# Kernel tuning notes

Hardware: AMD Instinct MI355X
Metric: run time of the kernel (lower is better)

The kernel has to match this reference:

```python
import jax, jax.numpy as jnp
import numpy as np

B, T, D = 2, 1024, 384
d = D // 3            # 128
D3 = 3 * d            # 384
D9 = 9 * d            # 1152
GAMMA = 5.0
EPS_W = 1e-8
EPS_N = 1e-5


def _orth(rng, n):
    q, _ = np.linalg.qr(rng.standard_normal((n, n)).astype(np.float64))
    return jnp.asarray(q.astype(np.float32))


def setup_inputs() -> dict:
    key = jax.random.key(0)
    x = jax.random.normal(key, (B, T, D), dtype=jnp.float32)
    rng = np.random.default_rng(0)
    def plin(fan_in, fan_out):
        W = jnp.asarray(rng.standard_normal((fan_out, fan_in)).astype(np.float32) * 0.05)
        b = jnp.zeros((fan_out,), jnp.float32)
        return W, b
    Wq, bq = plin(d, D3); Sq = _orth(rng, D3)
    Wk, bk = plin(d, D3); Sk = _orth(rng, D3)
    Wv, bv = plin(d, D3); Sv = _orth(rng, D3)
    Wp, bp = plin(D3, D9)
    gn = jnp.ones((D9,), jnp.float32)
    bn = jnp.zeros((D9,), jnp.float32)
    return {"x": x, "Wq": Wq, "bq": bq, "Sq": Sq, "Wk": Wk, "bk": bk, "Sk": Sk,
            "Wv": Wv, "bv": bv, "Sv": Sv, "Wp": Wp, "bp": bp, "gn": gn, "bn": bn}


def _plin(x, W, b):
    # PositiveLinearHK: linear with softplus-positive weights
    return x @ jax.nn.softplus(W).T + b


def reference(x, Wq, bq, Sq, Wk, bk, Sk, Wv, bv, Sv, Wp, bp, gn, bn):
    Q_base = x[:, :, 0 * d:1 * d]
    K_base = x[:, :, 1 * d:2 * d]
    V_base = x[:, :, 2 * d:3 * d]
    # proj = PositiveLinearHK -> SingleStiefelProjector (orthogonal mixing)
    Q = _plin(Q_base, Wq, bq) @ Sq          # (B,T,3d)
    K = _plin(K_base, Wk, bk) @ Sk
    V = _plin(V_base, Wv, bv) @ Sv
    dots = jnp.einsum('bti,btj->btij', Q, K)            # (B,T,3d,3d)
    scores = jax.nn.sigmoid(GAMMA * dots)
    weights = scores / (scores.sum(axis=-1, keepdims=True) + EPS_W)
    attended = jnp.einsum('btij,btj->bti', weights, V)  # (B,T,3d)
    h = _plin(attended, Wp, bp)                         # (B,T,9d)
    mu = h.mean(axis=-1, keepdims=True)
    var = h.var(axis=-1, keepdims=True)
    return (h - mu) * jax.lax.rsqrt(var + EPS_N) * gn + bn
```

## Files before the change

kernel.cpp:

```cpp
#include <hip/hip_runtime.h>
#include <hip/hip_bf16.h>
#include <math.h>

#define NTOK  2048
#define DD    128
#define DD3   384
#define DD9   1152
#define TB    2
#define TBP   8
#define GAMMA_F 5.0f
#define LN2_F   0.69314718f

#define OFF_M    0
#define OFF_C    147456
#define OFF_BP   148608
#define OFF_ATT  369792
#define OFF_SSUM 763008

typedef __attribute__((ext_vector_type(2))) float f32x2;
typedef __attribute__((ext_vector_type(8))) short bf16x8;
typedef __attribute__((ext_vector_type(4))) float f32x4;

__device__ __forceinline__ float softplusf(float x) {
    return fmaxf(x, 0.0f) + log1pf(__expf(-fabsf(x)));
}
__device__ __forceinline__ unsigned short f2bf(float f) {
    __hip_bfloat16 h = __float2bfloat16(f);
    return *reinterpret_cast<unsigned short*>(&h);
}
__device__ __forceinline__ float bf2f(unsigned short u) {
    return __uint_as_float(((unsigned)u) << 16);
}

__global__ __launch_bounds__(384) void k_prep(const float* __restrict__ Wq, const float* __restrict__ Wk,
                                              const float* __restrict__ Wv, const float* __restrict__ Wp,
                                              const float* __restrict__ Sq, const float* __restrict__ Sk,
                                              const float* __restrict__ Sv, const float* __restrict__ bq,
                                              const float* __restrict__ bk, const float* __restrict__ bv,
                                              float* __restrict__ ws) {
    __shared__ float sw[DD3];
    int b = blockIdx.x, tid = threadIdx.x;
    if (b < 576) {
        int idx = b * 384 + tid;
        unsigned lo = f2bf(softplusf(Wp[2 * idx + 0]) - LN2_F);
        unsigned hi = f2bf(softplusf(Wp[2 * idx + 1]) - LN2_F);
        ((unsigned*)(ws + OFF_BP))[idx] = lo | (hi << 16);
    } else if (b < 960) {
        int bb = b - 576;
        int mat = bb >> 7, i = bb & 127;
        const float* W = (mat == 0) ? Wq : (mat == 1 ? Wk : Wv);
        const float* S = (mat == 0) ? Sq : (mat == 1 ? Sk : Sv);
        int m = tid;
        sw[m] = softplusf(W[m * DD + i]);
        __syncthreads();
        const float4* sw4 = (const float4*)sw;
        float a0 = 0.f, a1 = 0.f, a2 = 0.f, a3 = 0.f;
        for (int j4 = 0; j4 < 96; ++j4) {
            float4 w = sw4[j4];
            int j = j4 * 4;
            a0 = fmaf(w.x, S[(j + 0) * DD3 + m], a0);
            a1 = fmaf(w.y, S[(j + 1) * DD3 + m], a1);
            a2 = fmaf(w.z, S[(j + 2) * DD3 + m], a2);
            a3 = fmaf(w.w, S[(j + 3) * DD3 + m], a3);
        }
        ws[OFF_M + mat * 49152 + (i >> 2) * (DD3 * 4) + m * 4 + (i & 3)] = (a0 + a1) + (a2 + a3);
    } else {
        int mat = b - 960;
        const float* S = (mat == 0) ? Sq : (mat == 1 ? Sk : Sv);
        const float* bb_ = (mat == 0) ? bq : (mat == 1 ? bk : bv);
        int m = tid;
        float a0 = 0.f, a1 = 0.f, a2 = 0.f, a3 = 0.f;
        for (int j4 = 0; j4 < 96; ++j4) {
            int j = j4 * 4;
            a0 = fmaf(bb_[j + 0], S[(j + 0) * DD3 + m], a0);
            a1 = fmaf(bb_[j + 1], S[(j + 1) * DD3 + m], a1);
            a2 = fmaf(bb_[j + 2], S[(j + 2) * DD3 + m], a2);
            a3 = fmaf(bb_[j + 3], S[(j + 3) * DD3 + m], a3);
        }
        ws[OFF_C + mat * DD3 + m] = (a0 + a1) + (a2 + a3);
    }
}

#define PSIG(FQ2, K2, V2, RS2, AV2) do {                                      \
        f32x2 x_ = __builtin_elementwise_min(                                  \
                     __builtin_elementwise_max((FQ2) * (K2), NEG1), POS1);     \
        f32x2 w_ = x_ * x_;                                                    \
        f32x2 p_ = __builtin_elementwise_fma(                                  \
                   __builtin_elementwise_fma(                                  \
                   __builtin_elementwise_fma(                                  \
                   __builtin_elementwise_fma(                                  \
                   __builtin_elementwise_fma(                                  \
                   __builtin_elementwise_fma(PC13, w_, PC11),                  \
                     w_, PC9), w_, PC7), w_, PC5), w_, PC3), w_, PC1);         \
        f32x2 s_ = __builtin_elementwise_fma(x_, p_, HALF2);                   \
        RS2 = RS2 + s_;                                                        \
        AV2 = __builtin_elementwise_fma(s_, (V2), AV2);                        \
    } while (0)

__global__ __launch_bounds__(384, 6) void k_attn(const float* __restrict__ x,
                                                 float* __restrict__ ws) {
    __shared__ float qkv[3 * TB * DD3];
    __shared__ float att[TB * DD3];
    __shared__ float red[16];

    int tid = threadIdx.x;
    int tok0 = blockIdx.x * TB;
    const float* xb = x + (size_t)tok0 * DD3;

#pragma unroll
    for (int mat = 0; mat < 3; ++mat) {
        const float4* M4 = (const float4*)(ws + OFF_M + mat * 49152);
        const float* xt0 = xb + 0 * DD3 + mat * DD;
        const float* xt1 = xb + 1 * DD3 + mat * DD;
        float a0 = 0.f, a1 = 0.f;
        for (int i4 = 0; i4 < 32; ++i4) {
            float4 mm = M4[i4 * DD3 + tid];
            int i = i4 * 4;
            a0 = fmaf(xt0[i], mm.x, fmaf(xt0[i + 1], mm.y, fmaf(xt0[i + 2], mm.z, fmaf(xt0[i + 3], mm.w, a0))));
            a1 = fmaf(xt1[i], mm.x, fmaf(xt1[i + 1], mm.y, fmaf(xt1[i + 2], mm.z, fmaf(xt1[i + 3], mm.w, a1))));
        }
        float c = ws[OFF_C + mat * DD3 + tid];
        qkv[(mat * TB + 0) * DD3 + tid] = a0 + c;
        qkv[(mat * TB + 1) * DD3 + tid] = a1 + c;
    }
    __syncthreads();

    {
        const f32x2 NEG1  = (f32x2){-1.0f, -1.0f};
        const f32x2 POS1  = (f32x2){ 1.0f,  1.0f};
        const f32x2 HALF2 = (f32x2){ 0.5f,  0.5f};
        const f32x2 PC1   = (f32x2){  1.4919730f,   1.4919730f};
        const f32x2 PC3   = (f32x2){ -4.1350490f,  -4.1350490f};
        const f32x2 PC5   = (f32x2){ 10.9501565f,  10.9501565f};
        const f32x2 PC7   = (f32x2){-20.0847165f, -20.0847165f};
        const f32x2 PC9   = (f32x2){ 22.6396415f,  22.6396415f};
        const f32x2 PC11  = (f32x2){-13.8982400f, -13.8982400f};
        const f32x2 PC13  = (f32x2){  3.5340290f,   3.5340290f};

        int t  = tid / 192;
        int ts = tid - t * 192;
        const float* Qt = qkv + t * DD3;
        float fq0s = Qt[ts]       * (GAMMA_F / 6.0f);
        float fq1s = Qt[ts + 192] * (GAMMA_F / 6.0f);
        f32x2 fq0 = (f32x2){fq0s, fq0s};
        f32x2 fq1 = (f32x2){fq1s, fq1s};
        const float4* K4 = (const float4*)(qkv + (TB + t) * DD3);
        const float4* V4 = (const float4*)(qkv + (2 * TB + t) * DD3);
        f32x2 rs0 = (f32x2){0.f, 0.f}, rs1 = (f32x2){0.f, 0.f};
        f32x2 av0 = (f32x2){0.f, 0.f}, av1 = (f32x2){0.f, 0.f};
        for (int j4 = 0; j4 < 96; ++j4) {
            float4 kk = K4[j4];
            float4 vv = V4[j4];
            f32x2 kxy = (f32x2){kk.x, kk.y}, kzw = (f32x2){kk.z, kk.w};
            f32x2 vxy = (f32x2){vv.x, vv.y}, vzw = (f32x2){vv.z, vv.w};
            PSIG(fq0, kxy, vxy, rs0, av0);
            PSIG(fq0, kzw, vzw, rs0, av0);
            PSIG(fq1, kxy, vxy, rs1, av1);
            PSIG(fq1, kzw, vzw, rs1, av1);
        }
        float a0 = (av0.x + av0.y) * __builtin_amdgcn_rcpf(rs0.x + rs0.y + 1e-8f);
        float a1 = (av1.x + av1.y) * __builtin_amdgcn_rcpf(rs1.x + rs1.y + 1e-8f);
        unsigned short b0 = f2bf(a0), b1 = f2bf(a1);
        att[t * DD3 + ts]       = bf2f(b0);
        att[t * DD3 + ts + 192] = bf2f(b1);
        unsigned short* ag = (unsigned short*)(ws + OFF_ATT);
        ag[(size_t)(tok0 + t) * DD3 + ts]       = b0;
        ag[(size_t)(tok0 + t) * DD3 + ts + 192] = b1;
    }
    __syncthreads();

    int wave = tid >> 6, lane64 = tid & 63;
    float s0 = att[0 * DD3 + tid];
    float s1 = att[1 * DD3 + tid];
#pragma unroll
    for (int off = 32; off; off >>= 1) {
        s0 += __shfl_down(s0, off, 64);
        s1 += __shfl_down(s1, off, 64);
    }
    if (lane64 == 0) { red[wave] = s0; red[8 + wave] = s1; }
    __syncthreads();
    if (tid < TB) {
        float a = 0.f;
        for (int w = 0; w < 6; ++w) a += red[tid * 8 + w];
        ws[OFF_SSUM + tok0 + tid] = a;
    }
}

__global__ __launch_bounds__(384) void k_proj(const float* __restrict__ bp,
                                              const float* __restrict__ gn,
                                              const float* __restrict__ bn,
                                              const float* __restrict__ ws,
                                              float* __restrict__ out) {
    __shared__ unsigned short attb[16 * 392];
    __shared__ float h[TBP * DD9];
    __shared__ float red[64];
    __shared__ float smu[TBP], sinv[TBP];

    int tid = threadIdx.x;
    int wave = tid >> 6, lane64 = tid & 63;
    int tok0 = blockIdx.x * TBP;

    {
        const unsigned short* ag = (const unsigned short*)(ws + OFF_ATT) + (size_t)tok0 * DD3;
        int r = tid / 48, c = (tid - r * 48) * 8;
        *(uint4*)(attb + r * 392 + c) = *(const uint4*)(ag + tid * 8);
        uint4 z; z.x = z.y = z.z = z.w = 0u;
        *(uint4*)(attb + (8 + r) * 392 + c) = z;
    }
    __syncthreads();

    {
        int n0w  = wave * 192;
        int brow = lane64 & 15;
        int koff = (lane64 >> 4) * 8;
        const unsigned short* Bp = (const unsigned short*)(ws + OFF_BP);
        const unsigned short* abase = attb + brow * 392 + koff;
        const unsigned short* bbase = Bp + (size_t)(n0w + brow) * DD3 + koff;
        f32x4 acc[12];
#pragma unroll
        for (int nt = 0; nt < 12; ++nt) acc[nt] = (f32x4){0.f, 0.f, 0.f, 0.f};
        for (int ks = 0; ks < 12; ++ks) {
            bf16x8 a = *(const bf16x8*)(abase + ks * 32);
            const unsigned short* bk_ = bbase + ks * 32;
#pragma unroll
            for (int nt = 0; nt < 12; ++nt) {
                bf16x8 bfr = *(const bf16x8*)(bk_ + nt * 16 * DD3);
                acc[nt] = __builtin_amdgcn_mfma_f32_16x16x32_bf16(a, bfr, acc[nt], 0, 0, 0);
            }
        }
        if (lane64 < 32) {
            int rbase = (lane64 >> 4) * 4;
            int col0  = n0w + (lane64 & 15);
#pragma unroll
            for (int nt = 0; nt < 12; ++nt) {
#pragma unroll
                for (int r = 0; r < 4; ++r)
                    h[(rbase + r) * DD9 + col0 + nt * 16] = acc[nt][r];
            }
        }
    }
    __syncthreads();

    const float* ssums = ws + OFF_SSUM + tok0;
    float acc3[3][TBP];
    {
        float bp0 = bp[tid], bp1 = bp[tid + DD3], bp2 = bp[tid + 2 * DD3];
#pragma unroll
        for (int t = 0; t < TBP; ++t) {
            float base = LN2_F * ssums[t];
            acc3[0][t] = h[t * DD9 + tid]           + bp0 + base;
            acc3[1][t] = h[t * DD9 + tid + DD3]     + bp1 + base;
            acc3[2][t] = h[t * DD9 + tid + 2 * DD3] + bp2 + base;
        }
    }
#pragma unroll
    for (int t = 0; t < TBP; ++t) {
        float s = acc3[0][t] + acc3[1][t] + acc3[2][t];
#pragma unroll
        for (int off = 32; off; off >>= 1) s += __shfl_down(s, off, 64);
        if (lane64 == 0) red[t * 8 + wave] = s;
    }
    __syncthreads();
    if (tid < TBP) {
        float a = 0.f;
        for (int w = 0; w < 6; ++w) a += red[tid * 8 + w];
        smu[tid] = a * (1.0f / 1152.0f);
    }
    __syncthreads();
#pragma unroll
    for (int t = 0; t < TBP; ++t) {
        float mu = smu[t];
        acc3[0][t] -= mu; acc3[1][t] -= mu; acc3[2][t] -= mu;
        float s = fmaf(acc3[0][t], acc3[0][t], fmaf(acc3[1][t], acc3[1][t], acc3[2][t] * acc3[2][t]));
#pragma unroll
        for (int off = 32; off; off >>= 1) s += __shfl_down(s, off, 64);
        if (lane64 == 0) red[t * 8 + wave] = s;
    }
    __syncthreads();
    if (tid < TBP) {
        float b = 0.f;
        for (int w = 0; w < 6; ++w) b += red[tid * 8 + w];
        sinv[tid] = __builtin_amdgcn_rsqf(b * (1.0f / 1152.0f) + 1e-5f);
    }
    __syncthreads();
    float g0 = gn[tid], g1 = gn[tid + DD3], g2 = gn[tid + 2 * DD3];
    float b0 = bn[tid], b1 = bn[tid + DD3], b2 = bn[tid + 2 * DD3];
#pragma unroll
    for (int t = 0; t < TBP; ++t) {
        float inv = sinv[t];
        size_t base = (size_t)(tok0 + t) * DD9;
        out[base + tid]           = fmaf(acc3[0][t] * inv, g0, b0);
        out[base + tid + DD3]     = fmaf(acc3[1][t] * inv, g1, b1);
        out[base + tid + 2 * DD3] = fmaf(acc3[2][t] * inv, g2, b2);
    }
}

extern "C" void kernel_launch(void* const* d_in, const int* in_sizes, int n_in,
                              void* d_out, int out_size, void* d_ws, size_t ws_size,
                              hipStream_t stream) {
    const float* x  = (const float*)d_in[0];
    const float* Wq = (const float*)d_in[1];
    const float* bq = (const float*)d_in[2];
    const float* Sq = (const float*)d_in[3];
    const float* Wk = (const float*)d_in[4];
    const float* bk = (const float*)d_in[5];
    const float* Sk = (const float*)d_in[6];
    const float* Wv = (const float*)d_in[7];
    const float* bv = (const float*)d_in[8];
    const float* Sv = (const float*)d_in[9];
    const float* Wp = (const float*)d_in[10];
    const float* bp = (const float*)d_in[11];
    const float* gn = (const float*)d_in[12];
    const float* bn = (const float*)d_in[13];
    float* out = (float*)d_out;
    float* ws  = (float*)d_ws;

    hipLaunchKernelGGL(k_prep, dim3(963), dim3(384), 0, stream,
                       Wq, Wk, Wv, Wp, Sq, Sk, Sv, bq, bk, bv, ws);
    hipLaunchKernelGGL(k_attn, dim3(NTOK / TB), dim3(384), 0, stream, x, ws);
    hipLaunchKernelGGL(k_proj, dim3(NTOK / TBP), dim3(384), 0, stream, bp, gn, bn, ws, out);
}
```

Baseline: 148.5 us.

## Split attention into separate QKV projection and sigmoid-attention kernels, batch prep rows

The fused attention kernel is split in two when the workspace is large enough. A QKV projection kernel handles 4 tokens per block and reuses each matrix load across more tokens, writing Q/K/V to global memory. A sigmoid-attention kernel reads them back, packs the two query elements per thread into one f32x2, and broadcasts K and V. The prep kernel now computes 8 rows of the fused W·S matrix per block instead of one, so each S load is reused 8 times. The cost is an extra kernel launch and a global round trip for QKV, and the new path only runs if the workspace size check passes.

Result: slower. 157.1 us (+5.8%).

```diff
diff --git a/kernel.cpp b/kernel.cpp
--- a/kernel.cpp
+++ b/kernel.cpp
@@ -7,6 +7,7 @@
 #define DD3   384
 #define DD9   1152
 #define TB    2
+#define TBQ   4
 #define TBP   8
 #define GAMMA_F 5.0f
 #define LN2_F   0.69314718f
@@ -16,7 +17,9 @@
 #define OFF_BP   148608
 #define OFF_ATT  369792
 #define OFF_SSUM 763008
-
+#define OFF_QKV  765056
+#define WS_NEED_SPLIT  ((size_t)3124352 * 4)
+  
 typedef __attribute__((ext_vector_type(2))) float f32x2;
 typedef __attribute__((ext_vector_type(8))) short bf16x8;
 typedef __attribute__((ext_vector_type(4))) float f32x4;
@@ -38,34 +41,42 @@
                                               const float* __restrict__ Sv, const float* __restrict__ bq,
                                               const float* __restrict__ bk, const float* __restrict__ bv,
                                               float* __restrict__ ws) {
-    __shared__ float sw[DD3];
+    __shared__ float sw[DD3 * 8];
     int b = blockIdx.x, tid = threadIdx.x;
     if (b < 576) {
         int idx = b * 384 + tid;
         unsigned lo = f2bf(softplusf(Wp[2 * idx + 0]) - LN2_F);
         unsigned hi = f2bf(softplusf(Wp[2 * idx + 1]) - LN2_F);
         ((unsigned*)(ws + OFF_BP))[idx] = lo | (hi << 16);
-    } else if (b < 960) {
+    } else if (b < 624) {
         int bb = b - 576;
-        int mat = bb >> 7, i = bb & 127;
+        int mat = bb >> 4, i0 = (bb & 15) * 8;
         const float* W = (mat == 0) ? Wq : (mat == 1 ? Wk : Wv);
         const float* S = (mat == 0) ? Sq : (mat == 1 ? Sk : Sv);
+#pragma unroll
+        for (int r = 0; r < 8; ++r)
+            sw[tid * 8 + r] = softplusf(W[tid * DD + i0 + r]);
+        __syncthreads();
         int m = tid;
-        sw[m] = softplusf(W[m * DD + i]);
-        __syncthreads();
+        float acc[8];
+#pragma unroll
+        for (int r = 0; r < 8; ++r) acc[r] = 0.f;
         const float4* sw4 = (const float4*)sw;
-        float a0 = 0.f, a1 = 0.f, a2 = 0.f, a3 = 0.f;
-        for (int j4 = 0; j4 < 96; ++j4) {
-            float4 w = sw4[j4];
-            int j = j4 * 4;
-            a0 = fmaf(w.x, S[(j + 0) * DD3 + m], a0);
-            a1 = fmaf(w.y, S[(j + 1) * DD3 + m], a1);
-            a2 = fmaf(w.z, S[(j + 2) * DD3 + m], a2);
-            a3 = fmaf(w.w, S[(j + 3) * DD3 + m], a3);
-        }
-        ws[OFF_M + mat * 49152 + (i >> 2) * (DD3 * 4) + m * 4 + (i & 3)] = (a0 + a1) + (a2 + a3);
+        for (int j = 0; j < DD3; ++j) {
+            float s = S[j * DD3 + m];
+            float4 w0 = sw4[j * 2], w1 = sw4[j * 2 + 1];
+            acc[0] = fmaf(w0.x, s, acc[0]); acc[1] = fmaf(w0.y, s, acc[1]);
+            acc[2] = fmaf(w0.z, s, acc[2]); acc[3] = fmaf(w0.w, s, acc[3]);
+            acc[4] = fmaf(w1.x, s, acc[4]); acc[5] = fmaf(w1.y, s, acc[5]);
+            acc[6] = fmaf(w1.z, s, acc[6]); acc[7] = fmaf(w1.w, s, acc[7]);
+        }
+#pragma unroll
+        for (int r = 0; r < 8; ++r) {
+            int i = i0 + r;
+            ws[OFF_M + mat * 49152 + (i >> 2) * (DD3 * 4) + m * 4 + (i & 3)] = acc[r];
+        }
     } else {
-        int mat = b - 960;
+        int mat = b - 624;
         const float* S = (mat == 0) ? Sq : (mat == 1 ? Sk : Sv);
         const float* bb_ = (mat == 0) ? bq : (mat == 1 ? bk : bv);
         int m = tid;
@@ -97,16 +108,110 @@
         AV2 = __builtin_elementwise_fma(s_, (V2), AV2);                        \
     } while (0)
 
+#define PSIG_CONSTS                                                            \
+    const f32x2 NEG1  = (f32x2){-1.0f, -1.0f};                                 \
+    const f32x2 POS1  = (f32x2){ 1.0f,  1.0f};                                 \
+    const f32x2 HALF2 = (f32x2){ 0.5f,  0.5f};                                 \
+    const f32x2 PC1   = (f32x2){  1.4919730f,   1.4919730f};                   \
+    const f32x2 PC3   = (f32x2){ -4.1350490f,  -4.1350490f};                   \
+    const f32x2 PC5   = (f32x2){ 10.9501565f,  10.9501565f};                   \
+    const f32x2 PC7   = (f32x2){-20.0847165f, -20.0847165f};                   \
+    const f32x2 PC9   = (f32x2){ 22.6396415f,  22.6396415f};                   \
+    const f32x2 PC11  = (f32x2){-13.8982400f, -13.8982400f};                   \
+    const f32x2 PC13  = (f32x2){  3.5340290f,   3.5340290f};
+
+__global__ __launch_bounds__(384, 3) void k_qkv(const float* __restrict__ x,
+                                                float* __restrict__ ws) {
+    int tid = threadIdx.x;
+    int tok0 = blockIdx.x * TBQ;
+    const float* xb = x + (size_t)tok0 * DD3;
+    float* qg = ws + OFF_QKV + (size_t)tok0 * DD9;
+#pragma unroll
+    for (int mat = 0; mat < 3; ++mat) {
+        const float4* M4 = (const float4*)(ws + OFF_M + mat * 49152);
+        const float* xt0 = xb + 0 * DD3 + mat * DD;
+        const float* xt1 = xb + 1 * DD3 + mat * DD;
+        const float* xt2 = xb + 2 * DD3 + mat * DD;
+        const float* xt3 = xb + 3 * DD3 + mat * DD;
+        float a0 = 0.f, a1 = 0.f, a2 = 0.f, a3 = 0.f;
+        for (int i4 = 0; i4 < 32; ++i4) {
+            float4 mm = M4[i4 * DD3 + tid];
+            int i = i4 * 4;
+            a0 = fmaf(xt0[i], mm.x, fmaf(xt0[i + 1], mm.y, fmaf(xt0[i + 2], mm.z, fmaf(xt0[i + 3], mm.w, a0))));
+            a1 = fmaf(xt1[i], mm.x, fmaf(xt1[i + 1], mm.y, fmaf(xt1[i + 2], mm.z, fmaf(xt1[i + 3], mm.w, a1))));
+            a2 = fmaf(xt2[i], mm.x, fmaf(xt2[i + 1], mm.y, fmaf(xt2[i + 2], mm.z, fmaf(xt2[i + 3], mm.w, a2))));
+            a3 = fmaf(xt3[i], mm.x, fmaf(xt3[i + 1], mm.y, fmaf(xt3[i + 2], mm.z, fmaf(xt3[i + 3], mm.w, a3))));
+        }
+        float c = ws[OFF_C + mat * DD3 + tid];
+        qg[0 * DD9 + mat * DD3 + tid] = a0 + c;
+        qg[1 * DD9 + mat * DD3 + tid] = a1 + c;
+        qg[2 * DD9 + mat * DD3 + tid] = a2 + c;
+        qg[3 * DD9 + mat * DD3 + tid] = a3 + c;
+    }
+}
+
+__global__ __launch_bounds__(384, 6) void k_sig(float* __restrict__ ws) {
+    __shared__ float att[TB * DD3];
+    __shared__ float red[16];
+    int tid = threadIdx.x;
+    int tok0 = blockIdx.x * TB;
+    int t  = __builtin_amdgcn_readfirstlane(tid / 192);
+    int ts = tid - t * 192;
+    const float* qkvg = ws + OFF_QKV + (size_t)(tok0 + t) * DD9;
+
+    PSIG_CONSTS
+    float fq0s = qkvg[ts]       * (GAMMA_F / 6.0f);
+    float fq1s = qkvg[ts + 192] * (GAMMA_F / 6.0f);
+    f32x2 fq2 = (f32x2){fq0s, fq1s};
+    const float* Kp = qkvg + DD3;
+    const float* Vp = qkvg + 2 * DD3;
+    f32x2 rs2 = (f32x2){0.f, 0.f}, av2 = (f32x2){0.f, 0.f};
+    for (int j0 = 0; j0 < DD3; j0 += 8) {
+        float ks[8], vs[8];
+#pragma unroll
+        for (int r = 0; r < 8; ++r) { ks[r] = Kp[j0 + r]; vs[r] = Vp[j0 + r]; }
+#pragma unroll
+        for (int r = 0; r < 8; ++r) {
+            f32x2 k2 = (f32x2){ks[r], ks[r]};
+            f32x2 v2 = (f32x2){vs[r], vs[r]};
+            PSIG(fq2, k2, v2, rs2, av2);
+        }
+    }
+    float a0 = av2.x * __builtin_amdgcn_rcpf(rs2.x + 1e-8f);
+    float a1 = av2.y * __builtin_amdgcn_rcpf(rs2.y + 1e-8f);
+    unsigned short b0 = f2bf(a0), b1 = f2bf(a1);
+    att[t * DD3 + ts]       = bf2f(b0);
+    att[t * DD3 + ts + 192] = bf2f(b1);
+    unsigned short* ag = (unsigned short*)(ws + OFF_ATT);
+    ag[(size_t)(tok0 + t) * DD3 + ts]       = b0;
+    ag[(size_t)(tok0 + t) * DD3 + ts + 192] = b1;
+    __syncthreads();
+
+    int wave = tid >> 6, lane64 = tid & 63;
+    float s0 = att[0 * DD3 + tid];
+    float s1 = att[1 * DD3 + tid];
+#pragma unroll
+    for (int off = 32; off; off >>= 1) {
+        s0 += __shfl_down(s0, off, 64);
+        s1 += __shfl_down(s1, off, 64);
+    }
+    if (lane64 == 0) { red[wave] = s0; red[8 + wave] = s1; }
+    __syncthreads();
+    if (tid < TB) {
+        float a = 0.f;
+        for (int w = 0; w < 6; ++w) a += red[tid * 8 + w];
+        ws[OFF_SSUM + tok0 + tid] = a;
+    }
+}
+
 __global__ __launch_bounds__(384, 6) void k_attn(const float* __restrict__ x,
                                                  float* __restrict__ ws) {
     __shared__ float qkv[3 * TB * DD3];
     __shared__ float att[TB * DD3];
     __shared__ float red[16];
-
     int tid = threadIdx.x;
     int tok0 = blockIdx.x * TB;
     const float* xb = x + (size_t)tok0 * DD3;
-
 #pragma unroll
     for (int mat = 0; mat < 3; ++mat) {
         const float4* M4 = (const float4*)(ws + OFF_M + mat * 49152);
@@ -124,19 +229,8 @@
         qkv[(mat * TB + 1) * DD3 + tid] = a1 + c;
     }
     __syncthreads();
-
     {
-        const f32x2 NEG1  = (f32x2){-1.0f, -1.0f};
-        const f32x2 POS1  = (f32x2){ 1.0f,  1.0f};
-        const f32x2 HALF2 = (f32x2){ 0.5f,  0.5f};
-        const f32x2 PC1   = (f32x2){  1.4919730f,   1.4919730f};
-        const f32x2 PC3   = (f32x2){ -4.1350490f,  -4.1350490f};
-        const f32x2 PC5   = (f32x2){ 10.9501565f,  10.9501565f};
-        const f32x2 PC7   = (f32x2){-20.0847165f, -20.0847165f};
-        const f32x2 PC9   = (f32x2){ 22.6396415f,  22.6396415f};
-        const f32x2 PC11  = (f32x2){-13.8982400f, -13.8982400f};
-        const f32x2 PC13  = (f32x2){  3.5340290f,   3.5340290f};
-
+        PSIG_CONSTS
         int t  = tid / 192;
         int ts = tid - t * 192;
         const float* Qt = qkv + t * DD3;
@@ -168,7 +262,6 @@
         ag[(size_t)(tok0 + t) * DD3 + ts + 192] = b1;
     }
     __syncthreads();
-
     int wave = tid >> 6, lane64 = tid & 63;
     float s0 = att[0 * DD3 + tid];
     float s1 = att[1 * DD3 + tid];
@@ -199,7 +292,6 @@
     int tid = threadIdx.x;
     int wave = tid >> 6, lane64 = tid & 63;
     int tok0 = blockIdx.x * TBP;
-
     {
         const unsigned short* ag = (const unsigned short*)(ws + OFF_ATT) + (size_t)tok0 * DD3;
         int r = tid / 48, c = (tid - r * 48) * 8;
@@ -208,7 +300,6 @@
         *(uint4*)(attb + (8 + r) * 392 + c) = z;
     }
     __syncthreads();
-
     {
         int n0w  = wave * 192;
         int brow = lane64 & 15;
@@ -315,8 +406,13 @@
     float* out = (float*)d_out;
     float* ws  = (float*)d_ws;
 
-    hipLaunchKernelGGL(k_prep, dim3(963), dim3(384), 0, stream,
+    hipLaunchKernelGGL(k_prep, dim3(627), dim3(384), 0, stream,
                        Wq, Wk, Wv, Wp, Sq, Sk, Sv, bq, bk, bv, ws);
-    hipLaunchKernelGGL(k_attn, dim3(NTOK / TB), dim3(384), 0, stream, x, ws);
+    if (ws_size >= WS_NEED_SPLIT) {
+        hipLaunchKernelGGL(k_qkv, dim3(NTOK / TBQ), dim3(384), 0, stream, x, ws);
+        hipLaunchKernelGGL(k_sig, dim3(NTOK / TB), dim3(384), 0, stream, ws);
+    } else {
+        hipLaunchKernelGGL(k_attn, dim3(NTOK / TB), dim3(384), 0, stream, x, ws);
+    }
     hipLaunchKernelGGL(k_proj, dim3(NTOK / TBP), dim3(384), 0, stream, bp, gn, bn, ws, out);
 }
```
